# Performance work log

Measured on AMD Instinct MI355X. Metric: run time of the kernel, lower is better.

The kernel has to match this reference:

```python
import jax, jax.numpy as jnp
import numpy as np

B, H, W, D = 8, 64, 64, 512
NH, DK = 16, 32
WS, SH = 8, 4            # window size, shift size = WS // 2
L = 4                    # n_layer
WS2 = WS * WS
NWH, NWW = H // WS, W // WS
SCALE = 1.0 / np.sqrt(DK)


def _rel_index(ws):
    # standard Swin relative position index: (ws^2, ws^2) into a (2ws-1)^2 table
    coords = np.stack(np.meshgrid(np.arange(ws), np.arange(ws), indexing='ij'))
    cf = coords.reshape(2, -1)
    rel = cf[:, :, None] - cf[:, None, :] + (ws - 1)
    return (rel[0] * (2 * ws - 1) + rel[1]).astype(np.int32)


def _shift_mask():
    # Swin-style shifted-window attention mask for cyclic shift by SH
    img = np.zeros((H, W), dtype=np.int32)
    cnt = 0
    sls = (slice(0, -WS), slice(-WS, -SH), slice(-SH, None))
    for hs in sls:
        for ws_ in sls:
            img[hs, ws_] = cnt
            cnt += 1
    win = img.reshape(NWH, WS, NWW, WS).transpose(0, 2, 1, 3).reshape(NWH, NWW, WS2)
    m = win[..., None, :] != win[..., :, None]          # (nh, nw, ws2, ws2)
    return np.broadcast_to(m[None, None], (1, NH, NWH, NWW, WS2, WS2)).copy()


def setup_inputs() -> dict:
    key = jax.random.key(0)
    ks = jax.random.split(key, 12)
    s = 0.02
    inp = {
        'x': jax.random.normal(ks[0], (B, H, W, D), jnp.float32),
        'mask': jnp.asarray(_shift_mask()),
        'rel_index': jnp.asarray(_rel_index(WS)),
        'Wq': jax.random.normal(ks[1], (L, D, D), jnp.float32) * s,
        'bq': jnp.zeros((L, D), jnp.float32),
        'Wkv': jax.random.normal(ks[2], (L, D, 2 * D), jnp.float32) * s,
        'bkv': jnp.zeros((L, 2 * D), jnp.float32),
        'Wo': jax.random.normal(ks[3], (L, D, D), jnp.float32) * s,
        'bo': jnp.zeros((L, D), jnp.float32),
        'rel_table': jax.random.normal(ks[4], (L, (2 * WS - 1) ** 2, NH), jnp.float32) * s,
        'ln1_g': jnp.ones((L, D), jnp.float32),
        'ln1_b': jnp.zeros((L, D), jnp.float32),
        'ln2_g': jnp.ones((L, D), jnp.float32),
        'ln2_b': jnp.zeros((L, D), jnp.float32),
        'W1': jax.random.normal(ks[5], (L, D, 4 * D), jnp.float32) * s,
        'b1': jnp.zeros((L, 4 * D), jnp.float32),
        'W2': jax.random.normal(ks[6], (L, 4 * D, D), jnp.float32) * s,
        'b2': jnp.zeros((L, D), jnp.float32),
    }
    return inp


def _ln(x, g, b):
    m = jnp.mean(x, -1, keepdims=True)
    v = jnp.mean(jnp.square(x - m), -1, keepdims=True)
    return (x - m) * jax.lax.rsqrt(v + 1e-5) * g + b


def _partition(t):
    # (B,H,W,NH,DK) -> (B,NH,nh,nw,ws^2,DK)
    t = t.reshape(B, NWH, WS, NWW, WS, NH, DK)
    return t.transpose(0, 5, 1, 3, 2, 4, 6).reshape(B, NH, NWH, NWW, WS2, DK)


def _merge(t):
    # (B,NH,nh,nw,ws^2,DK) -> (B,H,W,NH,DK)
    t = t.reshape(B, NH, NWH, NWW, WS, WS, DK).transpose(0, 2, 4, 3, 5, 1, 6)
    return t.reshape(B, H, W, NH, DK)


def _attn(xn, mask, rel_index, Wq, bq, Wkv, bkv, Wo, bo, table):
    q = (xn @ Wq + bq).reshape(B, H, W, NH, DK)
    kv = (xn @ Wkv + bkv).reshape(B, H, W, 2, NH, DK)
    k, v = kv[..., 0, :, :], kv[..., 1, :, :]
    # cyclic shift (shifting=True since n_class=4)
    q = jnp.roll(q, (-SH, -SH), axis=(1, 2))
    k = jnp.roll(k, (-SH, -SH), axis=(1, 2))
    v = jnp.roll(v, (-SH, -SH), axis=(1, 2))
    qw, kw, vw = _partition(q), _partition(k), _partition(v)
    scores = jnp.einsum('bhnmqd,bhnmkd->bhnmqk', qw, kw) * SCALE
    bias = table[rel_index]                      # (ws2, ws2, NH)
    scores = scores + bias.transpose(2, 0, 1)[None, :, None, None]
    scores = jnp.where(mask, -1e9, scores)
    a = jax.nn.softmax(scores, axis=-1)
    o = jnp.einsum('bhnmqk,bhnmkd->bhnmqd', a, vw)
    o = _merge(o)
    o = jnp.roll(o, (SH, SH), axis=(1, 2))       # reverse cyclic shift
    return o.reshape(B, H, W, D) @ Wo + bo


def reference(x, mask, rel_index, Wq, bq, Wkv, bkv, Wo, bo, rel_table,
              ln1_g, ln1_b, ln2_g, ln2_b, W1, b1, W2, b2):
    for i in range(L):
        x = x + _attn(_ln(x, ln1_g[i], ln1_b[i]), mask, rel_index,
                      Wq[i], bq[i], Wkv[i], bkv[i], Wo[i], bo[i], rel_table[i])
        h = _ln(x, ln2_g[i], ln2_b[i])
        x = x + (jax.nn.gelu(h @ W1[i] + b1[i]) @ W2[i] + b2[i])
    return x
```

## Files before the change

kernel.cpp:

```cpp
#include <hip/hip_runtime.h>
#include <hip/hip_bf16.h>

typedef __hip_bfloat16 bf16;
typedef __attribute__((ext_vector_type(8))) short short8;
typedef __attribute__((ext_vector_type(4))) float f32x4;

#define GLDS16(g, l) __builtin_amdgcn_global_load_lds(                              \
    (__attribute__((address_space(1))) const void*)(g),                             \
    (__attribute__((address_space(3))) void*)(l), 16, 0, 0)

#define SCALE_ 0.17677669529663687f

__global__ void detect_k(const unsigned int* __restrict__ ln1g_raw, int* __restrict__ flag)
{
    if (threadIdx.x == 0) *flag = (ln1g_raw[0] == 0x3F803F80u) ? 0 : 1;
}

__global__ __launch_bounds__(256)
void cvt_small_k(const void* __restrict__ src, bf16* __restrict__ dst, const int n,
                 const int* __restrict__ flag)
{
    const int i = blockIdx.x * 256 + threadIdx.x;
    if (i >= n) return;
    const bool f32 = (*flag != 0);
    dst[i] = f32 ? (bf16)((const float*)src)[i] : ((const bf16*)src)[i];
}

__global__ void transpose2_k(const float* __restrict__ inF, const bf16* __restrict__ inB,
                             bf16* __restrict__ out, const int R, const int C,
                             const int* __restrict__ flag)
{
    __shared__ bf16 tile[32][33];
    const bool f32 = (*flag != 0);
    const int c0 = blockIdx.x * 32, r0 = blockIdx.y * 32;
    const int tx = threadIdx.x, ty = threadIdx.y;
#pragma unroll
    for (int k = 0; k < 4; k++) {
        const long idx = (long)(r0 + ty + k * 8) * C + c0 + tx;
        tile[ty + k * 8][tx] = f32 ? (bf16)inF[idx] : inB[idx];
    }
    __syncthreads();
#pragma unroll
    for (int k = 0; k < 4; k++)
        out[(long)(c0 + ty + k * 8) * R + r0 + tx] = tile[tx][ty + k * 8];
}

__device__ __forceinline__ float gelu_f(float v)
{
    const float u = 0.7978845608028654f * (v + 0.044715f * v * v * v);
    const float e = __expf(-2.0f * u);
    return v * __builtin_amdgcn_rcpf(1.0f + e);
}

#define SBAR()   __builtin_amdgcn_s_barrier()
#define SCHED0() __builtin_amdgcn_sched_barrier(0)

template <int EPI>
__global__ __launch_bounds__(512, 2)
void gemm256(const bf16* __restrict__ A, const bf16* __restrict__ Bt,
             const bf16* __restrict__ bias0, const bf16* __restrict__ bias1,
             const int split,
             bf16* __restrict__ outb, float* __restrict__ outf,
             float* __restrict__ outf2,
             const int M, const int N, const int K)
{
    __shared__ char smem[131072] __attribute__((aligned(16)));

    const int nT  = N >> 8;
    const int nwg = gridDim.x;
    const int bid = blockIdx.x;
    const int wg = (bid & 7) * (nwg >> 3) + (bid >> 3);
    const int mb = wg / nT;
    const int nb = wg - mb * nT;
    const int m0 = mb << 8, n0 = nb << 8;

    const int tid  = threadIdx.x;
    const int lane = tid & 63;
    const int wave = tid >> 6;
    const int wm = wave >> 2;
    const int wn = wave & 3;
    const int fr  = lane & 15;
    const int oct = lane >> 4;
    const int l8  = lane >> 3;
    const int cx  = (lane & 7) ^ l8;

    const int T = K >> 6;

    const bf16* Asrc = A  + (long)(m0 + wm * 128 + wn * 32 + l8) * K + cx * 8;
    char*       Adst = smem + wm * 16384 + wn * 4096;
    const int h    = wn >> 1;
    const int bsub = wm * 2 + (wn & 1);
    const bf16* Bsrc = Bt + (long)(n0 + h * 128 + bsub * 32 + l8) * K + cx * 8;
    char*       Bdst = smem + 65536 + h * 16384 + bsub * 4096;

#define STAGE_A(kt, p) {                                                   \
        const bf16* s_ = Asrc + (long)(kt) * 64;                           \
        char* d_ = Adst + (p) * 32768;                                     \
        GLDS16(s_,            d_);                                         \
        GLDS16(s_ +  8L * K,  d_ + 1024);                                  \
        GLDS16(s_ + 16L * K,  d_ + 2048);                                  \
        GLDS16(s_ + 24L * K,  d_ + 3072); }
#define STAGE_B(kt, p) {                                                   \
        const bf16* s_ = Bsrc + (long)(kt) * 64;                           \
        char* d_ = Bdst + (p) * 32768;                                     \
        GLDS16(s_,            d_);                                         \
        GLDS16(s_ +  8L * K,  d_ + 1024);                                  \
        GLDS16(s_ + 16L * K,  d_ + 2048);                                  \
        GLDS16(s_ + 24L * K,  d_ + 3072); }

    const int kx0 = (     oct * 16) ^ ((fr & 7) << 4);
    const int kx1 = (64 + oct * 16) ^ ((fr & 7) << 4);
    const int aoff = (wm * 128 + fr) * 128;
    const int boff = 65536 + (wn * 64 + fr) * 128;

    f32x4 acc[8][4];
#pragma unroll
    for (int m = 0; m < 8; m++)
#pragma unroll
        for (int n = 0; n < 4; n++) acc[m][n] = (f32x4){0.f, 0.f, 0.f, 0.f};

    short8 af[4][2], bf[4][2];

    STAGE_B(0, 0); STAGE_A(0, 0);
    STAGE_B(1, 1); STAGE_A(1, 1);
    SCHED0();
    asm volatile("s_waitcnt vmcnt(8)");
    SCHED0();
    SBAR();

    for (int t = 0; t < T; ++t) {
        const int pOff = (t & 1) << 15;

#pragma unroll
        for (int mm = 0; mm < 4; mm++) {
            af[mm][0] = *(const short8*)(smem + pOff + aoff + mm * 2048 + kx0);
            af[mm][1] = *(const short8*)(smem + pOff + aoff + mm * 2048 + kx1);
        }
#pragma unroll
        for (int nn = 0; nn < 4; nn++) {
            bf[nn][0] = *(const short8*)(smem + pOff + boff + nn * 2048 + kx0);
            bf[nn][1] = *(const short8*)(smem + pOff + boff + nn * 2048 + kx1);
        }
        asm volatile("s_waitcnt lgkmcnt(0)");
        SCHED0();
        __builtin_amdgcn_s_setprio(1);
#pragma unroll
        for (int ks = 0; ks < 2; ks++)
#pragma unroll
            for (int mm = 0; mm < 4; mm++)
#pragma unroll
                for (int nn = 0; nn < 4; nn++)
                    acc[mm][nn] = __builtin_amdgcn_mfma_f32_16x16x32_bf16(
                        bf[nn][ks], af[mm][ks], acc[mm][nn], 0, 0, 0);
        __builtin_amdgcn_s_setprio(0);

#pragma unroll
        for (int mm = 0; mm < 4; mm++) {
            af[mm][0] = *(const short8*)(smem + pOff + aoff + (4 + mm) * 2048 + kx0);
            af[mm][1] = *(const short8*)(smem + pOff + aoff + (4 + mm) * 2048 + kx1);
        }
        asm volatile("s_waitcnt lgkmcnt(0)");
        SCHED0();
        __builtin_amdgcn_s_setprio(1);
#pragma unroll
        for (int ks = 0; ks < 2; ks++)
#pragma unroll
            for (int mm = 0; mm < 4; mm++)
#pragma unroll
                for (int nn = 0; nn < 4; nn++)
                    acc[4 + mm][nn] = __builtin_amdgcn_mfma_f32_16x16x32_bf16(
                        bf[nn][ks], af[mm][ks], acc[4 + mm][nn], 0, 0, 0);
        __builtin_amdgcn_s_setprio(0);

        SBAR();
        if (t < T - 2) { STAGE_B(t + 2, (t & 1)); STAGE_A(t + 2, (t & 1)); }
        SCHED0();
        if (t < T - 2)       { asm volatile("s_waitcnt vmcnt(8)"); }
        else if (t == T - 2) { asm volatile("s_waitcnt vmcnt(0)"); }
        SCHED0();
        SBAR();
    }
#undef STAGE_A
#undef STAGE_B

    if (EPI >= 2) {
        const int erow = m0 + wm * 128 + fr;
        const int ecol = n0 + wn * 64 + (oct << 2);
#pragma unroll
        for (int nn = 0; nn < 4; nn++) {
            const int col0 = ecol + nn * 16;
            const bf16* bp = (col0 < split) ? (bias0 + col0) : (bias1 + (col0 - split));
            const float bv0 = (float)bp[0], bv1 = (float)bp[1];
            const float bv2 = (float)bp[2], bv3 = (float)bp[3];
#pragma unroll
            for (int mm = 0; mm < 8; mm++) {
                const long base = (long)(erow + mm * 16) * N + col0;
                float4 o = *(const float4*)(outf + base);
                o.x += acc[mm][nn][0] + bv0;
                o.y += acc[mm][nn][1] + bv1;
                o.z += acc[mm][nn][2] + bv2;
                o.w += acc[mm][nn][3] + bv3;
                if (EPI == 2) *(float4*)(outf  + base) = o;
                else          *(float4*)(outf2 + base) = o;
            }
        }
    } else {
        const int col_l = wn * 64 + (oct << 2);
#pragma unroll
        for (int nn = 0; nn < 4; nn++) {
            const int cl = col_l + nn * 16;
            const int cg = n0 + cl;
            const bf16* bp = (cg < split) ? (bias0 + cg) : (bias1 + (cg - split));
            const float bv0 = (float)bp[0], bv1 = (float)bp[1];
            const float bv2 = (float)bp[2], bv3 = (float)bp[3];
#pragma unroll
            for (int mm = 0; mm < 8; mm++) {
                const int row_l = wm * 128 + mm * 16 + fr;
                float v0 = acc[mm][nn][0] + bv0;
                float v1 = acc[mm][nn][1] + bv1;
                float v2 = acc[mm][nn][2] + bv2;
                float v3 = acc[mm][nn][3] + bv3;
                if (EPI == 1) { v0 = gelu_f(v0); v1 = gelu_f(v1); v2 = gelu_f(v2); v3 = gelu_f(v3); }
                union { ushort4 u; bf16 hh[4]; } pk;
                pk.hh[0] = (bf16)v0; pk.hh[1] = (bf16)v1;
                pk.hh[2] = (bf16)v2; pk.hh[3] = (bf16)v3;
                int ad = (row_l << 9) + (cl << 1);
                ad ^= ((row_l & 7) << 4);
                *(ushort4*)(smem + ad) = pk.u;
            }
        }
        asm volatile("s_waitcnt lgkmcnt(0)");
        SBAR();
        const int rgrp = tid >> 5;
        const int chnk = tid & 31;
#pragma unroll
        for (int rr = 0; rr < 16; rr++) {
            const int row_l = rgrp * 16 + rr;
            int ad = (row_l << 9) + (chnk << 4);
            ad ^= ((row_l & 7) << 4);
            const uint4 val = *(const uint4*)(smem + ad);
            *(uint4*)((char*)outb + ((long)(m0 + row_l) * N + n0) * 2 + (chnk << 4)) = val;
        }
    }
}

__global__ __launch_bounds__(256)
void ln_k(const float* __restrict__ x, const bf16* __restrict__ g,
          const bf16* __restrict__ b, bf16* __restrict__ out)
{
    const int token = blockIdx.x * 4 + (threadIdx.x >> 6);
    const int lane  = threadIdx.x & 63;
    const float* xp = x + (long)token * 512 + lane * 8;
    float4 u0 = ((const float4*)xp)[0];
    float4 u1 = ((const float4*)xp)[1];
    float v[8] = {u0.x, u0.y, u0.z, u0.w, u1.x, u1.y, u1.z, u1.w};
    float s = 0.f, ss = 0.f;
#pragma unroll
    for (int e = 0; e < 8; e++) { s += v[e]; ss += v[e] * v[e]; }
#pragma unroll
    for (int off = 1; off < 64; off <<= 1) {
        s  += __shfl_xor(s,  off);
        ss += __shfl_xor(ss, off);
    }
    const float mean = s * (1.0f / 512.0f);
    const float var  = ss * (1.0f / 512.0f) - mean * mean;
    const float rstd = rsqrtf(var + 1e-5f);
    union { uint4 u; bf16 h[8]; } gg, bb, oo;
    gg.u = *(const uint4*)(g + lane * 8);
    bb.u = *(const uint4*)(b + lane * 8);
#pragma unroll
    for (int e = 0; e < 8; e++)
        oo.h[e] = (bf16)((v[e] - mean) * rstd * (float)gg.h[e] + (float)bb.h[e]);
    *(uint4*)(out + (long)token * 512 + lane * 8) = oo.u;
}

__global__ __launch_bounds__(256)
void lnx_k(const void* __restrict__ xin, const bf16* __restrict__ g,
           const bf16* __restrict__ b, float* __restrict__ xf,
           bf16* __restrict__ out, const int* __restrict__ flag)
{
    const int token = blockIdx.x * 4 + (threadIdx.x >> 6);
    const int lane  = threadIdx.x & 63;
    float v[8];
    if (*flag != 0) {
        const float* xp = (const float*)xin + (long)token * 512 + lane * 8;
        float4 u0 = ((const float4*)xp)[0];
        float4 u1 = ((const float4*)xp)[1];
        v[0] = u0.x; v[1] = u0.y; v[2] = u0.z; v[3] = u0.w;
        v[4] = u1.x; v[5] = u1.y; v[6] = u1.z; v[7] = u1.w;
    } else {
        union { uint4 u; bf16 h[8]; } t;
        t.u = *(const uint4*)((const bf16*)xin + (long)token * 512 + lane * 8);
#pragma unroll
        for (int e = 0; e < 8; e++) v[e] = (float)t.h[e];
    }
    float* xo = xf + (long)token * 512 + lane * 8;
    ((float4*)xo)[0] = make_float4(v[0], v[1], v[2], v[3]);
    ((float4*)xo)[1] = make_float4(v[4], v[5], v[6], v[7]);
    float s = 0.f, ss = 0.f;
#pragma unroll
    for (int e = 0; e < 8; e++) { s += v[e]; ss += v[e] * v[e]; }
#pragma unroll
    for (int off = 1; off < 64; off <<= 1) {
        s  += __shfl_xor(s,  off);
        ss += __shfl_xor(ss, off);
    }
    const float mean = s * (1.0f / 512.0f);
    const float var  = ss * (1.0f / 512.0f) - mean * mean;
    const float rstd = rsqrtf(var + 1e-5f);
    union { uint4 u; bf16 h[8]; } gg, bb, oo;
    gg.u = *(const uint4*)(g + lane * 8);
    bb.u = *(const uint4*)(b + lane * 8);
#pragma unroll
    for (int e = 0; e < 8; e++)
        oo.h[e] = (bf16)((v[e] - mean) * rstd * (float)gg.h[e] + (float)bb.h[e]);
    *(uint4*)(out + (long)token * 512 + lane * 8) = oo.u;
}

__global__ __launch_bounds__(64)
void bias_pre_k(const bf16* __restrict__ table, float* __restrict__ biasF)
{
    const int blk = blockIdx.x;
    const int q = blk & 63, n = (blk >> 6) & 15, c = blk >> 10;
    const int j = threadIdx.x;
    const int ri = q >> 3, ci = q & 7, rj = j >> 3, cj = j & 7;
    const float bias = (float)table[((ri - rj + 7) * 15 + (ci - cj + 7)) * 16 + n];
    const int shi = (c & 1) ? (ri < 4 ? 1 : 2) : 0;
    const int shj = (c & 1) ? (rj < 4 ? 1 : 2) : 0;
    const int swi = (c & 2) ? (ci < 4 ? 1 : 2) : 0;
    const int swj = (c & 2) ? (cj < 4 ? 1 : 2) : 0;
    biasF[((long)blk << 6) + j] = ((shi != shj) || (swi != swj)) ? -1.0e9f : bias;
}

__global__ __launch_bounds__(64, 3)
void attn_k2(const bf16* __restrict__ qkv, const float* __restrict__ biasF,
             bf16* __restrict__ out)
{
    __shared__ char lds[12800];
    const int bid = blockIdx.x;
    const int n  = bid & 15;
    const int ww = (bid >> 4) & 7;
    const int wh = (bid >> 7) & 7;
    const int b  = bid >> 10;
    const int lane = threadIdx.x;
    const int fr  = lane & 15;
    const int oct = lane >> 4;
    const int cls = ((wh == 7) ? 1 : 0) | ((ww == 7) ? 2 : 0);

    {
        const int d  = lane & 31;
        const int jh = lane >> 5;
        const long Ce = (((long)b * 64 + wh * 8 + 4) * 64 + (ww * 8 + 4)) * 1536;
        const long hsub = (wh == 7) ? 6291456L : 0L;
        const long wsub = (ww == 7) ? 98304L   : 0L;
        const long vbase = Ce + 1024 + n * 32 + d;
        long rowb[4];
#pragma unroll
        for (int qq = 0; qq < 4; qq++) {
            const int r = jh * 4 + qq;
            rowb[qq] = vbase + (long)r * 98304 - (r >= 4 ? hsub : 0);
        }
        union { ushort us[8]; uint4 u4; } vg[4];
#pragma unroll
        for (int c = 0; c < 32; c++) {
            const int qq = c >> 3, cj = c & 7;
            const long a = rowb[qq] + (long)cj * 1536 - (cj >= 4 ? wsub : 0);
            vg[qq].us[cj] = *(const ushort*)(qkv + a);
        }
#pragma unroll
        for (int qq = 0; qq < 4; qq++)
            *(uint4*)(lds + d * 144 + jh * 64 + qq * 16) = vg[qq].u4;
    }

    long tok[4];
#pragma unroll
    for (int tt = 0; tt < 4; tt++) {
        const int j = fr + 16 * tt;
        const int rj = j >> 3, cj = j & 7;
        const int gh = (wh * 8 + rj + 4) & 63;
        const int gw = (ww * 8 + cj + 4) & 63;
        tok[tt] = ((long)b * 64 + gh) * 64 + gw;
    }

    short8 kf[4];
#pragma unroll
    for (int t = 0; t < 4; t++)
        kf[t] = *(const short8*)(qkv + tok[t] * 1536 + 512 + n * 32 + oct * 8);

    const float* biasW = biasF + (((long)(cls * 16 + n)) << 12);
    float inv[4];
#pragma unroll
    for (int mm = 0; mm < 4; mm++) {
        const short8 qf = *(const short8*)(qkv + tok[mm] * 1536 + n * 32 + oct * 8);
        f32x4 sv[4];
#pragma unroll
        for (int nn = 0; nn < 4; nn++)
            sv[nn] = __builtin_amdgcn_mfma_f32_16x16x32_bf16(
                kf[nn], qf, (f32x4){0.f, 0.f, 0.f, 0.f}, 0, 0, 0);
        float p[16];
        float mx = -3.0e38f;
#pragma unroll
        for (int nn = 0; nn < 4; nn++) {
            const f32x4 bz = *(const f32x4*)(biasW + ((fr + 16 * mm) << 6) + nn * 16 + oct * 4);
#pragma unroll
            for (int r = 0; r < 4; r++) {
                p[nn * 4 + r] = sv[nn][r] * SCALE_ + bz[r];
                mx = fmaxf(mx, p[nn * 4 + r]);
            }
        }
        mx = fmaxf(mx, __shfl_xor(mx, 16));
        mx = fmaxf(mx, __shfl_xor(mx, 32));
        float sum = 0.f;
#pragma unroll
        for (int e = 0; e < 16; e++) { p[e] = __expf(p[e] - mx); sum += p[e]; }
        sum += __shfl_xor(sum, 16);
        sum += __shfl_xor(sum, 32);
        inv[mm] = __builtin_amdgcn_rcpf(sum);

        const int prow = 4608 + ((fr + 16 * mm) << 7);
#pragma unroll
        for (int nn = 0; nn < 4; nn++) {
            union { bf16 h[2]; unsigned u; } lo, hi;
            lo.h[0] = (bf16)p[nn * 4 + 0]; lo.h[1] = (bf16)p[nn * 4 + 1];
            hi.h[0] = (bf16)p[nn * 4 + 2]; hi.h[1] = (bf16)p[nn * 4 + 3];
            uint2 w; w.x = lo.u; w.y = hi.u;
            *(uint2*)(lds + prow + ((nn * 32 + oct * 8) ^ ((fr & 7) << 4))) = w;
        }
    }

    f32x4 oa[4][2];
#pragma unroll
    for (int mm = 0; mm < 4; mm++)
#pragma unroll
        for (int nd = 0; nd < 2; nd++) oa[mm][nd] = (f32x4){0.f, 0.f, 0.f, 0.f};
#pragma unroll
    for (int kc = 0; kc < 2; kc++) {
        const short8 vt0 = *(const short8*)(lds + fr * 144        + kc * 64 + oct * 16);
        const short8 vt1 = *(const short8*)(lds + (fr + 16) * 144 + kc * 64 + oct * 16);
#pragma unroll
        for (int mm = 0; mm < 4; mm++) {
            const short8 pf = *(const short8*)(lds + 4608 + ((fr + 16 * mm) << 7)
                                  + ((kc * 64 + oct * 16) ^ ((fr & 7) << 4)));
            oa[mm][0] = __builtin_amdgcn_mfma_f32_16x16x32_bf16(vt0, pf, oa[mm][0], 0, 0, 0);
            oa[mm][1] = __builtin_amdgcn_mfma_f32_16x16x32_bf16(vt1, pf, oa[mm][1], 0, 0, 0);
        }
    }

#pragma unroll
    for (int mm = 0; mm < 4; mm++) {
        bf16* op = out + tok[mm] * 512 + n * 32 + oct * 4;
#pragma unroll
        for (int nd = 0; nd < 2; nd++) {
            union { ushort4 u; bf16 h[4]; } o4;
#pragma unroll
            for (int r = 0; r < 4; r++) o4.h[r] = (bf16)(oa[mm][nd][r] * inv[mm]);
            *(ushort4*)(op + nd * 16) = o4.u;
        }
    }
}

extern "C" void kernel_launch(void* const* d_in, const int* in_sizes, int n_in,
                              void* d_out, int out_size, void* d_ws, size_t ws_size,
                              hipStream_t stream)
{
    const void* x_in = d_in[0];
    const void* Wq   = d_in[3];
    const void* bq   = d_in[4];
    const void* Wkv  = d_in[5];
    const void* bkv  = d_in[6];
    const void* Wo   = d_in[7];
    const void* bo   = d_in[8];
    const void* rtab = d_in[9];
    const void* ln1g = d_in[10];
    const void* ln1b = d_in[11];
    const void* ln2g = d_in[12];
    const void* ln2b = d_in[13];
    const void* W1   = d_in[14];
    const void* b1   = d_in[15];
    const void* W2   = d_in[16];
    const void* b2   = d_in[17];

    if (ws_size < (size_t)260046848) return;

    char* ws = (char*)d_ws;
    float* bufX   = (float*)(ws);
    bf16*  bufXN  = (bf16*)(ws + 67108864);
    bf16*  bufQKV = (bf16*)(ws + 100663296);
    bf16*  bufMLP = bufQKV;
    bf16*  bufATT = (bf16*)(ws + 201326592);
    bf16*  wT     = (bf16*)(ws + 234881024);
    bf16*  p_b2w  = (bf16*)(ws + 100663296 - 4096);

    int*  flag = (int*)d_out;
    bf16* pp   = (bf16*)((char*)d_out + 256);
    bf16* p_bq   = pp;
    bf16* p_bkv  = pp + 2048;
    bf16* p_bo   = pp + 6144;
    bf16* p_rtab = pp + 8192;
    bf16* p_l1g  = pp + 22592;
    bf16* p_l1b  = pp + 24640;
    bf16* p_l2g  = pp + 26688;
    bf16* p_l2b  = pp + 28736;
    bf16* p_b1   = pp + 30784;
    bf16* p_b2   = pp + 38976;
    float* biasAll = (float*)((char*)d_out + 33554432);

    const long LSTR = 3145728;

    detect_k<<<1, 64, 0, stream>>>((const unsigned int*)ln1g, flag);

    cvt_small_k<<<8,  256, 0, stream>>>(bq,   p_bq,   2048,  flag);
    cvt_small_k<<<16, 256, 0, stream>>>(bkv,  p_bkv,  4096,  flag);
    cvt_small_k<<<8,  256, 0, stream>>>(bo,   p_bo,   2048,  flag);
    cvt_small_k<<<57, 256, 0, stream>>>(rtab, p_rtab, 14400, flag);
    cvt_small_k<<<8,  256, 0, stream>>>(ln1g, p_l1g,  2048,  flag);
    cvt_small_k<<<8,  256, 0, stream>>>(ln1b, p_l1b,  2048,  flag);
    cvt_small_k<<<8,  256, 0, stream>>>(ln2g, p_l2g,  2048,  flag);
    cvt_small_k<<<8,  256, 0, stream>>>(ln2b, p_l2b,  2048,  flag);
    cvt_small_k<<<32, 256, 0, stream>>>(b1,   p_b1,   8192,  flag);
    cvt_small_k<<<8,  256, 0, stream>>>(b2,   p_b2,   2048,  flag);

    for (int i = 0; i < 4; i++)
        bias_pre_k<<<4096, 64, 0, stream>>>(p_rtab + i * 3600, biasAll + (long)i * 262144);

    for (int i = 0; i < 4; i++) {
        bf16* wl = wT + (long)i * LSTR;
        transpose2_k<<<dim3(16,16), dim3(32,8), 0, stream>>>(
            (const float*)Wq  + (long)i*262144,  (const bf16*)Wq  + (long)i*262144,
            wl,           512,  512, flag);
        transpose2_k<<<dim3(32,16), dim3(32,8), 0, stream>>>(
            (const float*)Wkv + (long)i*524288,  (const bf16*)Wkv + (long)i*524288,
            wl + 262144,  512, 1024, flag);
        transpose2_k<<<dim3(16,16), dim3(32,8), 0, stream>>>(
            (const float*)Wo  + (long)i*262144,  (const bf16*)Wo  + (long)i*262144,
            wl + 786432,  512,  512, flag);
        transpose2_k<<<dim3(64,16), dim3(32,8), 0, stream>>>(
            (const float*)W1  + (long)i*1048576, (const bf16*)W1  + (long)i*1048576,
            wl + 1048576, 512, 2048, flag);
        transpose2_k<<<dim3(16,64), dim3(32,8), 0, stream>>>(
            (const float*)W2  + (long)i*1048576, (const bf16*)W2  + (long)i*1048576,
            wl + 2097152, 2048, 512, flag);
    }

    for (int i = 0; i < 4; i++) {
        const bf16* wl = wT + (long)i * LSTR;
        if (i == 0)
            lnx_k<<<8192, 256, 0, stream>>>(x_in, p_l1g, p_l1b, bufX, bufXN, flag);
        else
            ln_k<<<8192, 256, 0, stream>>>(bufX, p_l1g + i*512, p_l1b + i*512, bufXN);
        gemm256<0><<<768, 512, 0, stream>>>(bufXN, wl, p_bq + i*512, p_bkv + i*1024, 512,
                                            bufQKV, nullptr, nullptr, 32768, 1536, 512);
        attn_k2<<<8192, 64, 0, stream>>>(bufQKV, biasAll + (long)i * 262144, bufATT);
        gemm256<2><<<256, 512, 0, stream>>>(bufATT, wl + 786432, p_bo + i*512, p_bo + i*512, 512,
                                            nullptr, bufX, nullptr, 32768, 512, 512);
        ln_k<<<8192, 256, 0, stream>>>(bufX, p_l2g + i*512, p_l2b + i*512, bufXN);
        gemm256<1><<<1024, 512, 0, stream>>>(bufXN, wl + 1048576, p_b1 + i*2048, p_b1 + i*2048, 2048,
                                             bufMLP, nullptr, nullptr, 32768, 2048, 512);
        if (i < 3) {
            gemm256<2><<<256, 512, 0, stream>>>(bufMLP, wl + 2097152, p_b2 + i*512, p_b2 + i*512, 512,
                                                nullptr, bufX, nullptr, 32768, 512, 2048);
        } else {
            cvt_small_k<<<8, 256, 0, stream>>>(b2, p_b2w, 2048, flag);
            gemm256<3><<<256, 512, 0, stream>>>(bufMLP, wl + 2097152, p_b2w + 1536, p_b2w + 1536, 512,
                                                nullptr, bufX, (float*)d_out, 32768, 512, 2048);
        }
    }
}
```

Measured before the change: 1.795 ms.

## Prefetch all LDS fragments per k-tile and overlap next global stage with MFMAs

The GEMM main loop now issues every LDS fragment read for a k-tile up front, using inline ds_read_b128 with immediate offsets and a second A register set. It waits only for the first half before starting MFMAs. The global-to-LDS staging of tile t+2 is issued before the second MFMA block instead of after both blocks, so memory traffic overlaps compute. The loop is unrolled by two to make the ping-pong buffer offsets compile-time constants. This raises register pressure and assumes T is even.

```diff
diff --git a/kernel.cpp b/kernel.cpp
--- a/kernel.cpp
+++ b/kernel.cpp
@@ -54,6 +54,9 @@
 
 #define SBAR()   __builtin_amdgcn_s_barrier()
 #define SCHED0() __builtin_amdgcn_sched_barrier(0)
+
+#define DSR(D, A, O) asm volatile("ds_read_b128 %0, %1 offset:%2" \
+                                  : "=v"(D) : "v"(A), "i"(O))
 
 template <int EPI>
 __global__ __launch_bounds__(512, 2)
@@ -113,13 +116,20 @@
     const int aoff = (wm * 128 + fr) * 128;
     const int boff = 65536 + (wn * 64 + fr) * 128;
 
+    const unsigned ldsbase =
+        (unsigned)(size_t)((__attribute__((address_space(3))) char*)smem);
+    const unsigned aA0 = ldsbase + aoff + kx0;
+    const unsigned aA1 = ldsbase + aoff + kx1;
+    const unsigned aB0 = ldsbase + boff + kx0;
+    const unsigned aB1 = ldsbase + boff + kx1;
+
     f32x4 acc[8][4];
 #pragma unroll
     for (int m = 0; m < 8; m++)
 #pragma unroll
         for (int n = 0; n < 4; n++) acc[m][n] = (f32x4){0.f, 0.f, 0.f, 0.f};
 
-    short8 af[4][2], bf[4][2];
+    short8 af[4][2], ag[4][2], bf[4][2];
 
     STAGE_B(0, 0); STAGE_A(0, 0);
     STAGE_B(1, 1); STAGE_A(1, 1);
@@ -128,58 +138,56 @@
     SCHED0();
     SBAR();
 
-    for (int t = 0; t < T; ++t) {
-        const int pOff = (t & 1) << 15;
-
-#pragma unroll
-        for (int mm = 0; mm < 4; mm++) {
-            af[mm][0] = *(const short8*)(smem + pOff + aoff + mm * 2048 + kx0);
-            af[mm][1] = *(const short8*)(smem + pOff + aoff + mm * 2048 + kx1);
-        }
-#pragma unroll
-        for (int nn = 0; nn < 4; nn++) {
-            bf[nn][0] = *(const short8*)(smem + pOff + boff + nn * 2048 + kx0);
-            bf[nn][1] = *(const short8*)(smem + pOff + boff + nn * 2048 + kx1);
-        }
-        asm volatile("s_waitcnt lgkmcnt(0)");
-        SCHED0();
-        __builtin_amdgcn_s_setprio(1);
-#pragma unroll
-        for (int ks = 0; ks < 2; ks++)
-#pragma unroll
-            for (int mm = 0; mm < 4; mm++)
-#pragma unroll
-                for (int nn = 0; nn < 4; nn++)
-                    acc[mm][nn] = __builtin_amdgcn_mfma_f32_16x16x32_bf16(
-                        bf[nn][ks], af[mm][ks], acc[mm][nn], 0, 0, 0);
-        __builtin_amdgcn_s_setprio(0);
-
-#pragma unroll
-        for (int mm = 0; mm < 4; mm++) {
-            af[mm][0] = *(const short8*)(smem + pOff + aoff + (4 + mm) * 2048 + kx0);
-            af[mm][1] = *(const short8*)(smem + pOff + aoff + (4 + mm) * 2048 + kx1);
-        }
-        asm volatile("s_waitcnt lgkmcnt(0)");
-        SCHED0();
-        __builtin_amdgcn_s_setprio(1);
-#pragma unroll
-        for (int ks = 0; ks < 2; ks++)
-#pragma unroll
-            for (int mm = 0; mm < 4; mm++)
-#pragma unroll
-                for (int nn = 0; nn < 4; nn++)
-                    acc[4 + mm][nn] = __builtin_amdgcn_mfma_f32_16x16x32_bf16(
-                        bf[nn][ks], af[mm][ks], acc[4 + mm][nn], 0, 0, 0);
-        __builtin_amdgcn_s_setprio(0);
-
-        SBAR();
-        if (t < T - 2) { STAGE_B(t + 2, (t & 1)); STAGE_A(t + 2, (t & 1)); }
-        SCHED0();
-        if (t < T - 2)       { asm volatile("s_waitcnt vmcnt(8)"); }
-        else if (t == T - 2) { asm volatile("s_waitcnt vmcnt(0)"); }
-        SCHED0();
-        SBAR();
-    }
+#define MFMA_BLK(F, MO)                                                       \
+    _Pragma("unroll")                                                         \
+    for (int ks = 0; ks < 2; ks++)                                            \
+      _Pragma("unroll")                                                       \
+      for (int mm = 0; mm < 4; mm++)                                          \
+        _Pragma("unroll")                                                     \
+        for (int nn = 0; nn < 4; nn++)                                        \
+            acc[(MO) + mm][nn] = __builtin_amdgcn_mfma_f32_16x16x32_bf16(     \
+                bf[nn][ks], F[mm][ks], acc[(MO) + mm][nn], 0, 0, 0);
+
+#define KTILE(POFF, KT)                                                       \
+  {                                                                           \
+    DSR(af[0][0], aA0, (POFF));          DSR(af[0][1], aA1, (POFF));          \
+    DSR(af[1][0], aA0, (POFF)+2048);     DSR(af[1][1], aA1, (POFF)+2048);     \
+    DSR(af[2][0], aA0, (POFF)+4096);     DSR(af[2][1], aA1, (POFF)+4096);     \
+    DSR(af[3][0], aA0, (POFF)+6144);     DSR(af[3][1], aA1, (POFF)+6144);     \
+    DSR(bf[0][0], aB0, (POFF));          DSR(bf[0][1], aB1, (POFF));          \
+    DSR(bf[1][0], aB0, (POFF)+2048);     DSR(bf[1][1], aB1, (POFF)+2048);     \
+    DSR(bf[2][0], aB0, (POFF)+4096);     DSR(bf[2][1], aB1, (POFF)+4096);     \
+    DSR(bf[3][0], aB0, (POFF)+6144);     DSR(bf[3][1], aB1, (POFF)+6144);     \
+    DSR(ag[0][0], aA0, (POFF)+8192);     DSR(ag[0][1], aA1, (POFF)+8192);     \
+    DSR(ag[1][0], aA0, (POFF)+10240);    DSR(ag[1][1], aA1, (POFF)+10240);    \
+    DSR(ag[2][0], aA0, (POFF)+12288);    DSR(ag[2][1], aA1, (POFF)+12288);    \
+    DSR(ag[3][0], aA0, (POFF)+14336);    DSR(ag[3][1], aA1, (POFF)+14336);    \
+    asm volatile("s_waitcnt lgkmcnt(8)");      \
+    SCHED0();                                                                 \
+    __builtin_amdgcn_s_setprio(1);                                            \
+    MFMA_BLK(af, 0)                                                           \
+    __builtin_amdgcn_s_setprio(0);                                            \
+    asm volatile("s_waitcnt lgkmcnt(0)");                    \
+    SCHED0();                                                                 \
+    SBAR();          \
+    if ((KT) < T - 2) { STAGE_B((KT) + 2, (KT) & 1); STAGE_A((KT) + 2, (KT) & 1); } \
+    SCHED0();                                                                 \
+    __builtin_amdgcn_s_setprio(1);                                            \
+    MFMA_BLK(ag, 4)                                                           \
+    __builtin_amdgcn_s_setprio(0);                                            \
+    SCHED0();                                                                 \
+    if ((KT) < T - 2)       { asm volatile("s_waitcnt vmcnt(8)"); }           \
+    else if ((KT) == T - 2) { asm volatile("s_waitcnt vmcnt(0)"); }           \
+    SCHED0();                                                                 \
+    SBAR();                              \
+  }
+
+    for (int t = 0; t < T; t += 2) {
+        KTILE(0, t);
+        KTILE(32768, t + 1);
+    }
+#undef KTILE
+#undef MFMA_BLK
 #undef STAGE_A
 #undef STAGE_B
 
```

Measured after the change: 2.025 ms. 12.8% more time.
